# Performance work log

Hardware: AMD Instinct MI355X
Metric: run time of the kernel (lower is better)

Reference implementation:

```python
import jax, jax.numpy as jnp
import numpy as np

N, E, B, ROWS, IN, HID, JKO, FEAT, OH, OUT = 200000, 6400000, 64, 128, 128, 6, 4, 2560, 20, 2

def _leaky(x, s):
    return jnp.where(x >= 0, x, s * x)

def _ln(x, g, b, eps=1e-5):
    mu = jnp.mean(x, -1, keepdims=True)
    v = jnp.mean((x - mu) ** 2, -1, keepdims=True)
    return (x - mu) * jax.lax.rsqrt(v + eps) * g + b

def setup_inputs():
    key = jax.random.key(0)
    ks = jax.random.split(key, 32)
    def w(k, shape, fan_in):
        return jax.random.normal(k, shape, jnp.float32) * (1.0 / np.sqrt(fan_in))
    inp = {
        'x': jax.random.normal(ks[0], (N, IN), jnp.float32),
        'edge_index': jax.random.randint(ks[1], (2, E), 0, N, jnp.int32),
        'batch': jnp.sort(jax.random.randint(ks[2], (N,), 0, B, jnp.int32)),
        'features': jax.random.normal(ks[3], (B, ROWS, FEAT), jnp.float32),
        'one_hot': jax.random.uniform(ks[4], (B, OH), jnp.float32),
        # GATv2Conv params (heads=1)
        'W_l': w(ks[5], (IN, HID), IN), 'b_l': jnp.zeros((HID,)),
        'W_r': w(ks[6], (IN, HID), IN), 'b_r': jnp.zeros((HID,)),
        'att': w(ks[7], (HID,), HID), 'conv_b': jnp.zeros((HID,)),
        # BasicGNN final lin after JK (6 -> 4)
        'jk_W': w(ks[8], (HID, JKO), HID), 'jk_b': jnp.zeros((JKO,)),
        # MLP chain on features
        'l1_W': w(ks[9], (FEAT, 256), FEAT), 'l1_b': jnp.zeros((256,)),
        'ln1_g': jnp.ones((256,)), 'ln1_b': jnp.zeros((256,)),
        'l2_W': w(ks[10], (256, 64), 256), 'l2_b': jnp.zeros((64,)),
        'ln2_g': jnp.ones((64,)), 'ln2_b': jnp.zeros((64,)),
        'l3_W': w(ks[11], (64, 8), 64), 'l3_b': jnp.zeros((8,)),
        'ln3_g': jnp.ones((8,)), 'ln3_b': jnp.zeros((8,)),
        # flattening: rows*8 -> 32
        'fl_W': w(ks[12], (ROWS * 8, 32), ROWS * 8), 'fl_b': jnp.zeros((32,)),
        'ln4_g': jnp.ones((32,)), 'ln4_b': jnp.zeros((32,)),
        # output: 4 + 32 + 20 = 56 -> OUT
        'out_W': w(ks[13], (56, OUT), 56), 'out_b': jnp.zeros((OUT,)),
    }
    return inp

def _forward(x, features, one_hot, W_l, b_l, W_r, b_r, att, conv_b, jk_W, jk_b,
             l1_W, l1_b, ln1_g, ln1_b, l2_W, l2_b, ln2_g, ln2_b, l3_W, l3_b, ln3_g, ln3_b,
             fl_W, fl_b, ln4_g, ln4_b, out_W, out_b, edge_index, batch):
    n = x.shape[0]
    # GATv2Conv, heads=1: separate source/target transforms
    xl = x @ W_l + b_l  # [N,6] source/message features
    xr = x @ W_r + b_r  # [N,6] target features
    loops = jnp.arange(n, dtype=edge_index.dtype)
    src = jnp.concatenate([edge_index[0], loops])  # add self loops
    dst = jnp.concatenate([edge_index[1], loops])
    e = _leaky(xl[src] + xr[dst], 0.2)             # [E+N,6]
    score = e @ att                                 # [E+N]
    m = jax.lax.stop_gradient(jax.ops.segment_max(score, dst, num_segments=n))
    p = jnp.exp(score - m[dst])
    z = jax.ops.segment_sum(p, dst, num_segments=n)
    alpha = p / z[dst]                              # segment softmax over incoming edges
    agg = jax.ops.segment_sum(alpha[:, None] * xl[src], dst, num_segments=n) + conv_b
    x1 = _leaky(agg, 0.01)                          # BasicGNN act ('leakyrelu')
    # JK-LSTM with a single layer collapses to identity (softmax over 1 element)
    h = x1 @ jk_W + jk_b                            # [N,4]
    # global mean pool per graph
    nb = features.shape[0]
    sums = jax.ops.segment_sum(h, batch, num_segments=nb)
    cnt = jax.ops.segment_sum(jnp.ones((n,), h.dtype), batch, num_segments=nb)
    xgcn = sums / jnp.maximum(cnt, 1.0)[:, None]    # [B,4]
    # MLP on features (dropout = identity in eval)
    f = _leaky(_ln(features @ l1_W + l1_b, ln1_g, ln1_b), 0.01)
    f = _leaky(_ln(f @ l2_W + l2_b, ln2_g, ln2_b), 0.01)
    f = _leaky(_ln(f @ l3_W + l3_b, ln3_g, ln3_b), 0.01)  # [B,ROWS,8]
    flat = f.reshape(nb, -1)
    xf = _leaky(_ln(flat @ fl_W + fl_b, ln4_g, ln4_b), 0.01)  # [B,32]
    cat = jnp.concatenate([xgcn, xf, one_hot], axis=1)        # [B,56]
    return cat @ out_W + out_b

def reference(x, features, one_hot, W_l, b_l, W_r, b_r, att, conv_b, jk_W, jk_b,
              l1_W, l1_b, ln1_g, ln1_b, l2_W, l2_b, ln2_g, ln2_b, l3_W, l3_b, ln3_g, ln3_b,
              fl_W, fl_b, ln4_g, ln4_b, out_W, out_b, edge_index, batch):
    return _forward(x, features, one_hot, W_l, b_l, W_r, b_r, att, conv_b, jk_W, jk_b,
                    l1_W, l1_b, ln1_g, ln1_b, l2_W, l2_b, ln2_g, ln2_b, l3_W, l3_b, ln3_g, ln3_b,
                    fl_W, fl_b, ln4_g, ln4_b, out_W, out_b, edge_index, batch)
```

## Files before the change

kernel.cpp:

```cpp
#include <hip/hip_runtime.h>
#include <cstdint>
#include <cstddef>

#define N_NODES 200000
#define N_EDGES 6400000
#define NB      64
#define MROWS   8192
#define FEAT    2560

#define BSZ   256
#define NBK   782
#define EBLK  512
#define ETILE 12500
#define BCAP  8960
#define NXB   768
#define GEMMB 256

typedef __attribute__((ext_vector_type(8))) short bf16x8;
typedef __attribute__((ext_vector_type(4))) float f32x4;

__device__ __forceinline__ unsigned short bf16rne(float f) {
    unsigned u = __builtin_bit_cast(unsigned, f);
    u += 0x7fffu + ((u >> 16) & 1u);
    return (unsigned short)(u >> 16);
}

__device__ __forceinline__ void async_cp16(const void* g, void* l) {
    __builtin_amdgcn_global_load_lds(
        (const __attribute__((address_space(1))) unsigned int*)g,
        (__attribute__((address_space(3))) unsigned int*)l, 16, 0, 0);
}

__device__ __forceinline__ void edge_acc(
    uint4 g, const float* xrd, const float* attv, float& z, float* agg)
{
    float xls[6];
    xls[0] = __builtin_bit_cast(float, g.x << 16);
    xls[1] = __builtin_bit_cast(float, g.x & 0xffff0000u);
    xls[2] = __builtin_bit_cast(float, g.y << 16);
    xls[3] = __builtin_bit_cast(float, g.y & 0xffff0000u);
    xls[4] = __builtin_bit_cast(float, g.z << 16);
    xls[5] = __builtin_bit_cast(float, g.z & 0xffff0000u);
    float sc = 0.f;
#pragma unroll
    for (int j = 0; j < 6; j++) {
        float e = xls[j] + xrd[j];
        e = (e >= 0.f) ? e : 0.2f * e;
        sc += attv[j] * e;
    }
    const float p = __expf(sc);
    z += p;
#pragma unroll
    for (int j = 0; j < 6; j++) agg[j] += p * xls[j];
}


__device__ __forceinline__ void nx_body(
    const int nxi, const int nstride,
    const float* __restrict__ x,
    const float* __restrict__ Wl, const float* __restrict__ bl,
    const float* __restrict__ Wr, const float* __restrict__ br,
    unsigned short* __restrict__ xlb, float* __restrict__ xr)
{
    const int t = threadIdx.x;
    const int l = t & 15;

    float wl[48], wr[48];
#pragma unroll
    for (int q = 0; q < 12; q++) {
        *(float4*)&wl[q * 4] = *(const float4*)(Wl + 48 * l + 4 * q);
        *(float4*)&wr[q * 4] = *(const float4*)(Wr + 48 * l + 4 * q);
    }
    for (int g = nxi; g < N_NODES / 16; g += nstride) {
        const int node = g * 16 + (t >> 4);
        float xv[8];
        *(float4*)&xv[0] = *(const float4*)(x + (size_t)node * 128 + l * 8);
        *(float4*)&xv[4] = *(const float4*)(x + (size_t)node * 128 + l * 8 + 4);

        float al[6] = {}, ar[6] = {};
#pragma unroll
        for (int i = 0; i < 8; i++) {
#pragma unroll
            for (int j = 0; j < 6; j++) {
                al[j] += xv[i] * wl[i * 6 + j];
                ar[j] += xv[i] * wr[i * 6 + j];
            }
        }
#pragma unroll
        for (int off = 8; off >= 1; off >>= 1) {
#pragma unroll
            for (int j = 0; j < 6; j++) {
                al[j] += __shfl_xor(al[j], off);
                ar[j] += __shfl_xor(ar[j], off);
            }
        }
        if (l == 0) {
            union { unsigned short h[8]; uint4 v; } u;
#pragma unroll
            for (int j = 0; j < 6; j++) u.h[j] = bf16rne(al[j] + bl[j]);
            u.h[6] = 0; u.h[7] = 0;
            *(uint4*)(xlb + (size_t)node * 8) = u.v;
            float4 r0; float2 r1;
            r0.x = ar[0] + br[0]; r0.y = ar[1] + br[1];
            r0.z = ar[2] + br[2]; r0.w = ar[3] + br[3];
            r1.x = ar[4] + br[4]; r1.y = ar[5] + br[5];
            *(float4*)(xr + (size_t)node * 8) = r0;
            *(float2*)(xr + (size_t)node * 8 + 4) = r1;
        }
    }
}

__device__ __forceinline__ void eb_body(
    const int bid, char* smem,
    const int* __restrict__ ei, int* __restrict__ cursor, int* __restrict__ pairs)
{
    int* sorted = (int*)smem;
    int* hb     = sorted + ETILE;
    int* cur    = hb + NBK + 1;
    int* gbl    = cur + NBK;
    int* wsum   = gbl + NBK;
    const int t = threadIdx.x;
    const int lane = t & 63, wid = t >> 6;
    const int base = bid * ETILE;

    for (int b = t; b < NBK; b += 256) cur[b] = 0;
    __syncthreads();

    for (int i = t; i < ETILE; i += 256)
        atomicAdd(&cur[ei[N_EDGES + base + i] >> 8], 1);
    __syncthreads();

    int c[4]; int lsum = 0;
#pragma unroll
    for (int q = 0; q < 4; q++) {
        const int b = 4 * t + q;
        c[q] = (b < NBK) ? cur[b] : 0;
        lsum += c[q];
    }
    int v = lsum;
#pragma unroll
    for (int d = 1; d < 64; d <<= 1) {
        const int o = __shfl_up(v, d);
        if (lane >= d) v += o;
    }
    if (lane == 63) wsum[wid] = v;
    __syncthreads();
    int off = 0;
#pragma unroll
    for (int w = 0; w < 3; w++) if (w < wid) off += wsum[w];
    int run = off + v - lsum;

    int mygb[4];
#pragma unroll
    for (int q = 0; q < 4; q++) {
        const int b = 4 * t + q;
        mygb[q] = (b < NBK && c[q] > 0) ? atomicAdd(&cursor[b], c[q]) : 0;
    }

#pragma unroll
    for (int q = 0; q < 4; q++) {
        const int b = 4 * t + q;
        if (b <= NBK) hb[b] = run;
        if (b < NBK) cur[b] = run;
        run += c[q];
    }
    __syncthreads();

    for (int i = t; i < ETILE; i += 256) {
        const int d = ei[N_EDGES + base + i];
        const int s = ei[base + i];
        const int pos = atomicAdd(&cur[d >> 8], 1);
        sorted[pos] = (s << 8) | (d & 255);
    }
#pragma unroll
    for (int q = 0; q < 4; q++) {
        const int b = 4 * t + q;
        if (b < NBK) gbl[b] = mygb[q];
    }
    __syncthreads();

    const int grp = t >> 4, gl = t & 15;
    for (int b = grp; b < NBK; b += 16) {
        const int st = hb[b];
        const int cnt = hb[b + 1] - st;
        int* dst = pairs + b * BCAP + gbl[b];
        for (int i = gl; i < cnt; i += 16)
            dst[i] = sorted[st + i];
    }
}

__device__ __forceinline__ void gemm_l1_body(
    const int bx, const int by, char* smem,
    const float* __restrict__ A, const unsigned short* __restrict__ Bt,
    const float* __restrict__ bias, float* __restrict__ C)
{
    unsigned short (*As)[64 * 64] = (unsigned short(*)[64 * 64])smem;
    unsigned short (*Bs)[128 * 64] =
        (unsigned short(*)[128 * 64])(smem + 2 * 64 * 64 * sizeof(short));
    const int K = FEAT, N = 256;
    const int t = threadIdx.x;
    const int w = t >> 6, l = t & 63;
    const int l15 = l & 15, quad = l >> 4;
    const int wm = (w & 1) * 32, wn = (w >> 1) * 64;
    const int gm0 = bx * 64;
    const int gn0 = by * 128;
    const int r8 = l >> 3;
    const int c8 = (l & 7) ^ r8;
    const int ar = t >> 2;
    const int ac0 = (t & 3) * 2;

    f32x4 acc[2][4];
#pragma unroll
    for (int mt = 0; mt < 2; mt++)
#pragma unroll
        for (int nt = 0; nt < 4; nt++) acc[mt][nt] = (f32x4){0.f, 0.f, 0.f, 0.f};

    const int niter = K / 64;

#pragma unroll
    for (int c = 0; c < 4; c++) {
        const int j = w * 4 + c;
        async_cp16(Bt + (size_t)(gn0 + j * 8 + r8) * K + c8 * 8, &Bs[0][j * 512]);
    }
    {
        const float* src = A + (size_t)(gm0 + ar) * K + ac0 * 8;
        float4 v0 = *(const float4*)src;
        float4 v1 = *(const float4*)(src + 4);
        float4 v2 = *(const float4*)(src + 8);
        float4 v3 = *(const float4*)(src + 12);
        union { unsigned short h[8]; uint4 u; } p0, p1;
        p0.h[0] = bf16rne(v0.x); p0.h[1] = bf16rne(v0.y);
        p0.h[2] = bf16rne(v0.z); p0.h[3] = bf16rne(v0.w);
        p0.h[4] = bf16rne(v1.x); p0.h[5] = bf16rne(v1.y);
        p0.h[6] = bf16rne(v1.z); p0.h[7] = bf16rne(v1.w);
        p1.h[0] = bf16rne(v2.x); p1.h[1] = bf16rne(v2.y);
        p1.h[2] = bf16rne(v2.z); p1.h[3] = bf16rne(v2.w);
        p1.h[4] = bf16rne(v3.x); p1.h[5] = bf16rne(v3.y);
        p1.h[6] = bf16rne(v3.z); p1.h[7] = bf16rne(v3.w);
        *(uint4*)&As[0][ar * 64 + ((ac0 + 0) ^ (ar & 7)) * 8] = p0.u;
        *(uint4*)&As[0][ar * 64 + ((ac0 + 1) ^ (ar & 7)) * 8] = p1.u;
    }

    int p = 0;
    for (int i = 0; i < niter; i++) {
        __syncthreads();
        const bool nxt = (i + 1 < niter);
        float4 v0, v1, v2, v3;
        if (nxt) {
            const int k1 = (i + 1) * 64;
#pragma unroll
            for (int c = 0; c < 4; c++) {
                const int j = w * 4 + c;
                async_cp16(Bt + (size_t)(gn0 + j * 8 + r8) * K + k1 + c8 * 8,
                           &Bs[p ^ 1][j * 512]);
            }
            const float* src = A + (size_t)(gm0 + ar) * K + k1 + ac0 * 8;
            v0 = *(const float4*)src;
            v1 = *(const float4*)(src + 4);
            v2 = *(const float4*)(src + 8);
            v3 = *(const float4*)(src + 12);
        }
#pragma unroll
        for (int kki = 0; kki < 2; kki++) {
            bf16x8 af[2], bfr[4];
#pragma unroll
            for (int mt = 0; mt < 2; mt++) {
                const int m = wm + mt * 16 + l15;
                af[mt] = *(const bf16x8*)&As[p][m * 64 + (((quad + 4 * kki) ^ (m & 7)) * 8)];
            }
#pragma unroll
            for (int nt = 0; nt < 4; nt++) {
                const int n = wn + nt * 16 + l15;
                bfr[nt] = *(const bf16x8*)&Bs[p][n * 64 + (((quad + 4 * kki) ^ (n & 7)) * 8)];
            }
#pragma unroll
            for (int mt = 0; mt < 2; mt++)
#pragma unroll
                for (int nt = 0; nt < 4; nt++)
                    acc[mt][nt] = __builtin_amdgcn_mfma_f32_16x16x32_bf16(
                        af[mt], bfr[nt], acc[mt][nt], 0, 0, 0);
        }
        if (nxt) {
            union { unsigned short h[8]; uint4 u; } p0, p1;
            p0.h[0] = bf16rne(v0.x); p0.h[1] = bf16rne(v0.y);
            p0.h[2] = bf16rne(v0.z); p0.h[3] = bf16rne(v0.w);
            p0.h[4] = bf16rne(v1.x); p0.h[5] = bf16rne(v1.y);
            p0.h[6] = bf16rne(v1.z); p0.h[7] = bf16rne(v1.w);
            p1.h[0] = bf16rne(v2.x); p1.h[1] = bf16rne(v2.y);
            p1.h[2] = bf16rne(v2.z); p1.h[3] = bf16rne(v2.w);
            p1.h[4] = bf16rne(v3.x); p1.h[5] = bf16rne(v3.y);
            p1.h[6] = bf16rne(v3.z); p1.h[7] = bf16rne(v3.w);
            *(uint4*)&As[p ^ 1][ar * 64 + ((ac0 + 0) ^ (ar & 7)) * 8] = p0.u;
            *(uint4*)&As[p ^ 1][ar * 64 + ((ac0 + 1) ^ (ar & 7)) * 8] = p1.u;
        }
        p ^= 1;
    }
#pragma unroll
    for (int nt = 0; nt < 4; nt++) {
        const int col = gn0 + wn + nt * 16 + l15;
        const float bv = bias[col];
#pragma unroll
        for (int mt = 0; mt < 2; mt++)
#pragma unroll
            for (int rr = 0; rr < 4; rr++) {
                const int row = gm0 + wm + mt * 16 + quad * 4 + rr;
                C[(size_t)row * N + col] = acc[mt][nt][rr] + bv;
            }
    }
}


__global__ __launch_bounds__(256) void node_xform(
    const float* __restrict__ x,
    const float* __restrict__ Wl, const float* __restrict__ bl,
    const float* __restrict__ Wr, const float* __restrict__ br,
    unsigned short* __restrict__ xlb, float* __restrict__ xr)
{
    nx_body(blockIdx.x, N_NODES / 16, x, Wl, bl, Wr, br, xlb, xr);
}

__global__ __launch_bounds__(256) void edge_bucket(
    const int* __restrict__ ei, int* __restrict__ cursor, int* __restrict__ pairs)
{
    __shared__ __align__(16) char smem[59408];
    eb_body(blockIdx.x, smem, ei, cursor, pairs);
}

__global__ __launch_bounds__(256) void mfma_gemm_l1(
    const float* __restrict__ A, const unsigned short* __restrict__ Bt,
    const float* __restrict__ bias, float* __restrict__ C)
{
    __shared__ __align__(16) char smem[49152];
    gemm_l1_body(blockIdx.x, blockIdx.y, smem, A, Bt, bias, C);
}

__global__ __launch_bounds__(256) void fused_front(
    const float* __restrict__ x,
    const float* __restrict__ Wl, const float* __restrict__ bl,
    const float* __restrict__ Wr, const float* __restrict__ br,
    unsigned short* __restrict__ xlb, float* __restrict__ xr,
    const int* __restrict__ ei, int* __restrict__ cursor, int* __restrict__ pairs,
    const float* __restrict__ A, const unsigned short* __restrict__ Bt,
    const float* __restrict__ bias, float* __restrict__ C)
{
    __shared__ __align__(16) char smem[59408];
    const int bid = blockIdx.x;
    const int role = bid % 3;
    const int q = bid / 3;
    if (role == 0) {
        eb_body(q, smem, ei, cursor, pairs);
    } else if (role == 1 && q < GEMMB) {
        gemm_l1_body(q & 127, q >> 7, smem, A, Bt, bias, C);
    } else {
        const int nxi = (role == 2) ? q : EBLK + (q - GEMMB);
        nx_body(nxi, NXB, x, Wl, bl, Wr, br, xlb, xr);
    }
}

__global__ __launch_bounds__(256) void bucket_reduce(
    const int* __restrict__ pairs, const int* __restrict__ cursor,
    const unsigned short* __restrict__ xlb, const float* __restrict__ xr,
    const float* __restrict__ att, const float* __restrict__ conv_b,
    const float* __restrict__ jkW, const float* __restrict__ jkb,
    const int* __restrict__ batch,
    float* __restrict__ gsum, float* __restrict__ gcnt)
{
    __shared__ int sorted[BCAP];
    __shared__ int hist[256];
    __shared__ int wtot[4];
    const int t = threadIdx.x;
    const int lane = t & 63, wid = t >> 6;
    const int d0 = blockIdx.x * BSZ + t;

    float xrd[6];
    if (d0 < N_NODES) {
        float4 a = *(const float4*)(xr + (size_t)d0 * 8);
        float2 b = *(const float2*)(xr + (size_t)d0 * 8 + 4);
        xrd[0] = a.x; xrd[1] = a.y; xrd[2] = a.z;
        xrd[3] = a.w; xrd[4] = b.x; xrd[5] = b.y;
    } else {
#pragma unroll
        for (int j = 0; j < 6; j++) xrd[j] = 0.f;
    }
    float attv[6];
#pragma unroll
    for (int j = 0; j < 6; j++) attv[j] = att[j];

    float z = 0.f, agg[6] = {};
    const uint4* xl4 = (const uint4*)xlb;
    const int e0 = blockIdx.x * BCAP;
    const int e1 = e0 + cursor[blockIdx.x];

    for (int c0 = e0; c0 < e1; c0 += BCAP) {
        const int rem = e1 - c0;
        const int cnt_chunk = (rem < BCAP) ? rem : BCAP;
        hist[t] = 0;
        __syncthreads();
        for (int i = t; i < cnt_chunk; i += 256)
            atomicAdd(&hist[pairs[c0 + i] & 255], 1);
        __syncthreads();
        const int h = hist[t];
        int v = h;
#pragma unroll
        for (int d = 1; d < 64; d <<= 1) {
            int o = __shfl_up(v, d);
            if (lane >= d) v += o;
        }
        if (lane == 63) wtot[wid] = v;
        __syncthreads();
        int off = 0;
#pragma unroll
        for (int wv = 0; wv < 3; wv++) if (wv < wid) off += wtot[wv];
        const int my_start = v - h + off;
        const int my_cnt = h;
        __syncthreads();
        hist[t] = my_start;
        __syncthreads();
        for (int i = t; i < cnt_chunk; i += 256) {
            const int pv = pairs[c0 + i];
            const int pos = atomicAdd(&hist[pv & 255], 1);
            sorted[pos] = ((unsigned)pv) >> 8;
        }
        __syncthreads();
        int i = 0;
        for (; i + 4 <= my_cnt; i += 4) {
            const int s0 = sorted[my_start + i];
            const int s1 = sorted[my_start + i + 1];
            const int s2 = sorted[my_start + i + 2];
            const int s3 = sorted[my_start + i + 3];
            const uint4 g0 = xl4[s0], g1 = xl4[s1], g2 = xl4[s2], g3 = xl4[s3];
            edge_acc(g0, xrd, attv, z, agg);
            edge_acc(g1, xrd, attv, z, agg);
            edge_acc(g2, xrd, attv, z, agg);
            edge_acc(g3, xrd, attv, z, agg);
        }
        for (; i < my_cnt; i++) {
            const uint4 g = xl4[sorted[my_start + i]];
            edge_acc(g, xrd, attv, z, agg);
        }
        __syncthreads();
    }

    float hh[4] = {0.f, 0.f, 0.f, 0.f};
    float cw = 0.f;
    int b = 0;
    if (d0 < N_NODES) {
        const uint4 g = xl4[d0];
        float xld[6];
        xld[0] = __builtin_bit_cast(float, g.x << 16);
        xld[1] = __builtin_bit_cast(float, g.x & 0xffff0000u);
        xld[2] = __builtin_bit_cast(float, g.y << 16);
        xld[3] = __builtin_bit_cast(float, g.y & 0xffff0000u);
        xld[4] = __builtin_bit_cast(float, g.z << 16);
        xld[5] = __builtin_bit_cast(float, g.z & 0xffff0000u);
        float sc = 0.f;
#pragma unroll
        for (int j = 0; j < 6; j++) {
            float e = xld[j] + xrd[j];
            e = (e >= 0.f) ? e : 0.2f * e;
            sc += attv[j] * e;
        }
        const float p = __expf(sc);
        const float zz = z + p;
#pragma unroll
        for (int c = 0; c < 4; c++) hh[c] = jkb[c];
#pragma unroll
        for (int j = 0; j < 6; j++) {
            float aj = (agg[j] + p * xld[j]) / zz + conv_b[j];
            aj = (aj >= 0.f) ? aj : 0.01f * aj;
#pragma unroll
            for (int c = 0; c < 4; c++) hh[c] += aj * jkW[j * 4 + c];
        }
        b = batch[d0];
        cw = 1.f;
    }
    const int b0 = __shfl(b, 0);
    if (__all(b == b0)) {
#pragma unroll
        for (int off2 = 32; off2 >= 1; off2 >>= 1) {
#pragma unroll
            for (int c = 0; c < 4; c++) hh[c] += __shfl_xor(hh[c], off2);
            cw += __shfl_xor(cw, off2);
        }
        if (lane == 0 && cw > 0.f) {
#pragma unroll
            for (int c = 0; c < 4; c++) atomicAdd(gsum + b0 * 4 + c, hh[c]);
            atomicAdd(gcnt + b0, cw);
        }
    } else if (cw > 0.f) {
#pragma unroll
        for (int c = 0; c < 4; c++) atomicAdd(gsum + b * 4 + c, hh[c]);
        atomicAdd(gcnt + b, cw);
    }
}

__global__ __launch_bounds__(256) void castT(
    const float* __restrict__ W, unsigned short* __restrict__ Wt, int K, int N)
{
    const int k = blockIdx.x * 256 + threadIdx.x;
    const int n = blockIdx.y;
    if (k < K) Wt[(size_t)n * K + k] = bf16rne(W[(size_t)k * N + n]);
}

__global__ __launch_bounds__(256) void mfma_gemm_l2(
    const unsigned short* __restrict__ Ab, const unsigned short* __restrict__ Bt,
    const float* __restrict__ bias, float* __restrict__ C,
    int M, int N, int K)
{
    __shared__ unsigned short As[32 * 64];
    __shared__ unsigned short Bs[64 * 64];
    const int t = threadIdx.x;
    const int w = t >> 6, l = t & 63;
    const int l15 = l & 15, quad = l >> 4;
    const int gm0 = blockIdx.x * 32;
    const int gn0 = blockIdx.y * 64;
    const int r8 = l >> 3;
    const int c8 = (l & 7) ^ r8;

    f32x4 acc[2];
    acc[0] = (f32x4){0.f, 0.f, 0.f, 0.f};
    acc[1] = (f32x4){0.f, 0.f, 0.f, 0.f};

    for (int k0 = 0; k0 < K; k0 += 64) {
#pragma unroll
        for (int c = 0; c < 2; c++) {
            const int j = w * 2 + c;
            async_cp16(Bt + (size_t)(gn0 + j * 8 + r8) * K + k0 + c8 * 8,
                       &Bs[j * 512]);
        }
        async_cp16(Ab + (size_t)(gm0 + w * 8 + r8) * K + k0 + c8 * 8, &As[w * 512]);
        __syncthreads();
#pragma unroll
        for (int kki = 0; kki < 2; kki++) {
            bf16x8 af[2], bfr;
#pragma unroll
            for (int mt = 0; mt < 2; mt++) {
                const int m = mt * 16 + l15;
                af[mt] = *(const bf16x8*)&As[m * 64 + (((quad + 4 * kki) ^ (m & 7)) * 8)];
            }
            const int n = w * 16 + l15;
            bfr = *(const bf16x8*)&Bs[n * 64 + (((quad + 4 * kki) ^ (n & 7)) * 8)];
#pragma unroll
            for (int mt = 0; mt < 2; mt++)
                acc[mt] = __builtin_amdgcn_mfma_f32_16x16x32_bf16(
                    af[mt], bfr, acc[mt], 0, 0, 0);
        }
        __syncthreads();
    }
    const int col = gn0 + w * 16 + l15;
    const float bv = bias[col];
#pragma unroll
    for (int mt = 0; mt < 2; mt++)
#pragma unroll
        for (int rr = 0; rr < 4; rr++) {
            const int row = gm0 + mt * 16 + quad * 4 + rr;
            C[(size_t)row * N + col] = acc[mt][rr] + bv;
        }
}

__global__ __launch_bounds__(256) void ln_leaky_c256(
    const float* __restrict__ f, unsigned short* __restrict__ out,
    const float* __restrict__ g, const float* __restrict__ b)
{
    const int row = blockIdx.x;
    const int t = threadIdx.x;
    float v = f[(size_t)row * 256 + t];
    float s = v, s2 = v * v;
#pragma unroll
    for (int off = 32; off >= 1; off >>= 1) {
        s += __shfl_xor(s, off);
        s2 += __shfl_xor(s2, off);
    }
    __shared__ float ws[4], ws2[4];
    const int wid = t >> 6, lane = t & 63;
    if (lane == 0) { ws[wid] = s; ws2[wid] = s2; }
    __syncthreads();
    const float S = ws[0] + ws[1] + ws[2] + ws[3];
    const float S2 = ws2[0] + ws2[1] + ws2[2] + ws2[3];
    const float mu = S * (1.0f / 256.0f);
    const float var = S2 * (1.0f / 256.0f) - mu * mu;
    float y = (v - mu) * rsqrtf(var + 1e-5f) * g[t] + b[t];
    y = (y >= 0.f) ? y : 0.01f * y;
    out[(size_t)row * 256 + t] = bf16rne(y);
}

__global__ __launch_bounds__(256) void ln_leaky_c64(
    float* __restrict__ f, const float* __restrict__ g, const float* __restrict__ b)
{
    const int wid = threadIdx.x >> 6, lane = threadIdx.x & 63;
    const int row = blockIdx.x * 4 + wid;
    float v = f[(size_t)row * 64 + lane];
    float s = v, s2 = v * v;
#pragma unroll
    for (int off = 32; off >= 1; off >>= 1) {
        s += __shfl_xor(s, off);
        s2 += __shfl_xor(s2, off);
    }
    const float mu = s * (1.0f / 64.0f);
    const float var = s2 * (1.0f / 64.0f) - mu * mu;
    float y = (v - mu) * rsqrtf(var + 1e-5f) * g[lane] + b[lane];
    f[(size_t)row * 64 + lane] = (y >= 0.f) ? y : 0.01f * y;
}

__global__ __launch_bounds__(256) void l3_ln_leaky(
    const float* __restrict__ f2, const float* __restrict__ W3,
    const float* __restrict__ b3,
    const float* __restrict__ g, const float* __restrict__ b,
    float* __restrict__ f3)
{
    __shared__ float sW[64 * 8];
    const int t = threadIdx.x;
    sW[t] = W3[t]; sW[t + 256] = W3[t + 256];
    __syncthreads();
    const int row = blockIdx.x * 32 + (t >> 3);
    const int c = t & 7;
    float acc = b3[c];
    const float* fr = f2 + (size_t)row * 64;
#pragma unroll 8
    for (int k = 0; k < 64; k++) acc += fr[k] * sW[k * 8 + c];
    float s = acc, s2 = acc * acc;
#pragma unroll
    for (int off = 4; off >= 1; off >>= 1) {
        s += __shfl_xor(s, off);
        s2 += __shfl_xor(s2, off);
    }
    const float mu = s * (1.0f / 8.0f);
    const float var = s2 * (1.0f / 8.0f) - mu * mu;
    float y = (acc - mu) * rsqrtf(var + 1e-5f) * g[c] + b[c];
    f3[(size_t)row * 8 + c] = (y >= 0.f) ? y : 0.01f * y;
}

__global__ __launch_bounds__(256) void flat_ln_leaky(
    const float* __restrict__ f3, const float* __restrict__ W,
    const float* __restrict__ bb,
    const float* __restrict__ g, const float* __restrict__ b,
    float* __restrict__ xf)
{
    __shared__ float sf[1024];
    __shared__ float sp[8][32];
    const int t = threadIdx.x;
    const int gb = blockIdx.x;
    *(float4*)&sf[t * 4] = *(const float4*)(f3 + (size_t)gb * 1024 + t * 4);
    __syncthreads();
    const int c = t & 31, part = t >> 5;
    float acc = 0.f;
    for (int k = part * 128; k < part * 128 + 128; k++) acc += sf[k] * W[k * 32 + c];
    sp[part][c] = acc;
    __syncthreads();
    if (t < 32) {
        float v = bb[t];
#pragma unroll
        for (int p = 0; p < 8; p++) v += sp[p][t];
        float s = v, s2 = v * v;
#pragma unroll
        for (int off = 16; off >= 1; off >>= 1) {
            s += __shfl_xor(s, off);
            s2 += __shfl_xor(s2, off);
        }
        const float mu = s * (1.0f / 32.0f);
        const float var = s2 * (1.0f / 32.0f) - mu * mu;
        float y = (v - mu) * rsqrtf(var + 1e-5f) * g[t] + b[t];
        xf[gb * 32 + t] = (y >= 0.f) ? y : 0.01f * y;
    }
}

__global__ __launch_bounds__(128) void final_out(
    const float* __restrict__ gsum, const float* __restrict__ gcnt,
    const float* __restrict__ xf, const float* __restrict__ onehot,
    const float* __restrict__ Wo, const float* __restrict__ bo,
    float* __restrict__ out)
{
    const int t = threadIdx.x;
    const int gb = t >> 1, o = t & 1;
    float cnt = gcnt[gb];
    cnt = (cnt > 1.f) ? cnt : 1.f;
    float acc = bo[o];
#pragma unroll
    for (int j = 0; j < 4; j++)  acc += (gsum[gb * 4 + j] / cnt) * Wo[j * 2 + o];
#pragma unroll
    for (int j = 0; j < 32; j++) acc += xf[gb * 32 + j] * Wo[(4 + j) * 2 + o];
#pragma unroll
    for (int j = 0; j < 20; j++) acc += onehot[gb * 20 + j] * Wo[(36 + j) * 2 + o];
    out[t] = acc;
}

extern "C" void kernel_launch(void* const* d_in, const int* in_sizes, int n_in,
                              void* d_out, int out_size, void* d_ws, size_t ws_size,
                              hipStream_t stream)
{
    const float* x        = (const float*)d_in[0];
    const int*   ei       = (const int*)d_in[1];
    const int*   batch    = (const int*)d_in[2];
    const float* features = (const float*)d_in[3];
    const float* one_hot  = (const float*)d_in[4];
    const float* W_l   = (const float*)d_in[5];
    const float* b_l   = (const float*)d_in[6];
    const float* W_r   = (const float*)d_in[7];
    const float* b_r   = (const float*)d_in[8];
    const float* att   = (const float*)d_in[9];
    const float* conv_b = (const float*)d_in[10];
    const float* jk_W  = (const float*)d_in[11];
    const float* jk_b  = (const float*)d_in[12];
    const float* l1_W  = (const float*)d_in[13];
    const float* l1_b  = (const float*)d_in[14];
    const float* ln1_g = (const float*)d_in[15];
    const float* ln1_b = (const float*)d_in[16];
    const float* l2_W  = (const float*)d_in[17];
    const float* l2_b  = (const float*)d_in[18];
    const float* ln2_g = (const float*)d_in[19];
    const float* ln2_b = (const float*)d_in[20];
    const float* l3_W  = (const float*)d_in[21];
    const float* l3_b  = (const float*)d_in[22];
    const float* ln3_g = (const float*)d_in[23];
    const float* ln3_b = (const float*)d_in[24];
    const float* fl_W  = (const float*)d_in[25];
    const float* fl_b  = (const float*)d_in[26];
    const float* ln4_g = (const float*)d_in[27];
    const float* ln4_b = (const float*)d_in[28];
    const float* out_W = (const float*)d_in[29];
    const float* out_b = (const float*)d_in[30];
    (void)in_sizes; (void)n_in; (void)out_size;

    float* ws = (float*)d_ws;
    unsigned short* xlb = (unsigned short*)(ws + 0);
    float* xr   = ws + 800000;
    unsigned short* w1t = (unsigned short*)(ws + 2400000);
    unsigned short* w2t = (unsigned short*)(ws + 2727680);
    float* gsum   = ws + 2735872;
    float* gcnt   = ws + 2736128;
    int*   cursor = (int*)(ws + 2736192);
    int* pairs = (int*)(ws + 2737024);

    const bool fuse = ws_size >= (size_t)13481344 * 4;
    float* f1;  unsigned short* f1b;  float* f2;  float* f3;  float* xf;
    if (fuse) {
        f1  = ws + 9743744;
        f1b = (unsigned short*)(ws + 11840896);
        f2  = ws + 12889472;
        f3  = ws + 13413760;
        xf  = ws + 13479296;
    } else {
        f1  = ws + 2737024;
        f1b = (unsigned short*)(ws + 4834176);
        f2  = ws + 5358464;
        f3  = ws + 5882752;
        xf  = ws + 5948288;
    }

    hipMemsetAsync(gsum, 0, 1102 * sizeof(float), stream);

    castT<<<dim3(10, 256), 256, 0, stream>>>(l1_W, w1t, FEAT, 256);
    castT<<<dim3(1, 64), 256, 0, stream>>>(l2_W, w2t, 256, 64);

    if (fuse) {
        fused_front<<<EBLK + GEMMB + NXB, 256, 0, stream>>>(
            x, W_l, b_l, W_r, b_r, xlb, xr,
            ei, cursor, pairs,
            features, w1t, l1_b, f1);
        bucket_reduce<<<NBK, 256, 0, stream>>>(pairs, cursor, xlb, xr, att,
                                               conv_b, jk_W, jk_b, batch,
                                               gsum, gcnt);
    } else {
        node_xform<<<N_NODES / 16, 256, 0, stream>>>(x, W_l, b_l, W_r, b_r,
                                                     xlb, xr);
        edge_bucket<<<EBLK, 256, 0, stream>>>(ei, cursor, pairs);
        bucket_reduce<<<NBK, 256, 0, stream>>>(pairs, cursor, xlb, xr, att,
                                               conv_b, jk_W, jk_b, batch,
                                               gsum, gcnt);
        mfma_gemm_l1<<<dim3(MROWS / 64, 2), 256, 0, stream>>>(
            features, w1t, l1_b, f1);
    }

    ln_leaky_c256<<<MROWS, 256, 0, stream>>>(f1, f1b, ln1_g, ln1_b);
    mfma_gemm_l2<<<dim3(MROWS / 32, 1), 256, 0, stream>>>(
        f1b, w2t, l2_b, f2, MROWS, 64, 256);
    ln_leaky_c64<<<MROWS / 4, 256, 0, stream>>>(f2, ln2_g, ln2_b);
    l3_ln_leaky<<<MROWS / 32, 256, 0, stream>>>(f2, l3_W, l3_b, ln3_g, ln3_b, f3);
    flat_ln_leaky<<<NB, 256, 0, stream>>>(f3, fl_W, fl_b, ln4_g, ln4_b, xf);
    final_out<<<1, 128, 0, stream>>>(gsum, gcnt, xf, one_hot, out_W, out_b, (float*)d_out);
}
```

Baseline: 541.7 us.

## Fuse MLP tail into per-graph blocks co-scheduled with bucket reduce

Replaces the chain of separate LN/GEMM-l2/LN/l3/flatten kernels with one per-graph MLP block that does LN1, the 256x64 layer in fp32 using bf16 weights held in LDS, LN2, l3+LN3 and the flatten layer entirely on-chip. These 64 MLP blocks are interleaved with the bucket_reduce blocks in a single fused_back launch, so the small MLP work overlaps the edge aggregation. This removes several launches and the f1b/f2/f3 round trips through memory. In exchange the l2 GEMM moves from MFMA to scalar shuffle-based FMA, and each MLP block processes 128 rows serially, so a slow MLP block could become the tail of fused_back.

```diff
diff --git a/kernel.cpp b/kernel.cpp
--- a/kernel.cpp
+++ b/kernel.cpp
@@ -15,6 +15,7 @@
 #define BCAP  8960
 #define NXB   768
 #define GEMMB 256
+#define MLPB  64
 
 typedef __attribute__((ext_vector_type(8))) short bf16x8;
 typedef __attribute__((ext_vector_type(4))) float f32x4;
@@ -23,6 +24,10 @@
     unsigned u = __builtin_bit_cast(unsigned, f);
     u += 0x7fffu + ((u >> 16) & 1u);
     return (unsigned short)(u >> 16);
+}
+
+__device__ __forceinline__ float bf16f(unsigned short h) {
+    return __builtin_bit_cast(float, (unsigned)h << 16);
 }
 
 __device__ __forceinline__ void async_cp16(const void* g, void* l) {
@@ -309,55 +314,8 @@
     }
 }
 
-
-__global__ __launch_bounds__(256) void node_xform(
-    const float* __restrict__ x,
-    const float* __restrict__ Wl, const float* __restrict__ bl,
-    const float* __restrict__ Wr, const float* __restrict__ br,
-    unsigned short* __restrict__ xlb, float* __restrict__ xr)
-{
-    nx_body(blockIdx.x, N_NODES / 16, x, Wl, bl, Wr, br, xlb, xr);
-}
-
-__global__ __launch_bounds__(256) void edge_bucket(
-    const int* __restrict__ ei, int* __restrict__ cursor, int* __restrict__ pairs)
-{
-    __shared__ __align__(16) char smem[59408];
-    eb_body(blockIdx.x, smem, ei, cursor, pairs);
-}
-
-__global__ __launch_bounds__(256) void mfma_gemm_l1(
-    const float* __restrict__ A, const unsigned short* __restrict__ Bt,
-    const float* __restrict__ bias, float* __restrict__ C)
-{
-    __shared__ __align__(16) char smem[49152];
-    gemm_l1_body(blockIdx.x, blockIdx.y, smem, A, Bt, bias, C);
-}
-
-__global__ __launch_bounds__(256) void fused_front(
-    const float* __restrict__ x,
-    const float* __restrict__ Wl, const float* __restrict__ bl,
-    const float* __restrict__ Wr, const float* __restrict__ br,
-    unsigned short* __restrict__ xlb, float* __restrict__ xr,
-    const int* __restrict__ ei, int* __restrict__ cursor, int* __restrict__ pairs,
-    const float* __restrict__ A, const unsigned short* __restrict__ Bt,
-    const float* __restrict__ bias, float* __restrict__ C)
-{
-    __shared__ __align__(16) char smem[59408];
-    const int bid = blockIdx.x;
-    const int role = bid % 3;
-    const int q = bid / 3;
-    if (role == 0) {
-        eb_body(q, smem, ei, cursor, pairs);
-    } else if (role == 1 && q < GEMMB) {
-        gemm_l1_body(q & 127, q >> 7, smem, A, Bt, bias, C);
-    } else {
-        const int nxi = (role == 2) ? q : EBLK + (q - GEMMB);
-        nx_body(nxi, NXB, x, Wl, bl, Wr, br, xlb, xr);
-    }
-}
-
-__global__ __launch_bounds__(256) void bucket_reduce(
+__device__ __forceinline__ void br_body(
+    const int bid, char* smem,
     const int* __restrict__ pairs, const int* __restrict__ cursor,
     const unsigned short* __restrict__ xlb, const float* __restrict__ xr,
     const float* __restrict__ att, const float* __restrict__ conv_b,
@@ -365,12 +323,12 @@
     const int* __restrict__ batch,
     float* __restrict__ gsum, float* __restrict__ gcnt)
 {
-    __shared__ int sorted[BCAP];
-    __shared__ int hist[256];
-    __shared__ int wtot[4];
+    int* sorted = (int*)smem;
+    int* hist   = sorted + BCAP;
+    int* wtot   = hist + 256;
     const int t = threadIdx.x;
     const int lane = t & 63, wid = t >> 6;
-    const int d0 = blockIdx.x * BSZ + t;
+    const int d0 = bid * BSZ + t;
 
     float xrd[6];
     if (d0 < N_NODES) {
@@ -388,8 +346,8 @@
 
     float z = 0.f, agg[6] = {};
     const uint4* xl4 = (const uint4*)xlb;
-    const int e0 = blockIdx.x * BCAP;
-    const int e1 = e0 + cursor[blockIdx.x];
+    const int e0 = bid * BCAP;
+    const int e1 = e0 + cursor[bid];
 
     for (int c0 = e0; c0 < e1; c0 += BCAP) {
         const int rem = e1 - c0;
@@ -494,6 +452,229 @@
     }
 }
 
+__device__ __forceinline__ void mlp_body(
+    const int g, char* smem,
+    const float* __restrict__ f1, const unsigned short* __restrict__ w2t,
+    const float* __restrict__ ln1_g, const float* __restrict__ ln1_b,
+    const float* __restrict__ l2_b,
+    const float* __restrict__ ln2_g, const float* __restrict__ ln2_b,
+    const float* __restrict__ l3_W, const float* __restrict__ l3_b,
+    const float* __restrict__ ln3_g, const float* __restrict__ ln3_b,
+    const float* __restrict__ fl_W, const float* __restrict__ fl_b,
+    const float* __restrict__ ln4_g, const float* __restrict__ ln4_b,
+    float* __restrict__ xf)
+{
+    unsigned short* W2 = (unsigned short*)smem;
+    float* f3s = (float*)(smem + 32768);
+    float* sp  = (float*)(smem + 32768 + 4096);
+    const int t = threadIdx.x;
+    const int w = t >> 6, l = t & 63;
+
+    for (int i = t; i < 16384; i += 256) {
+        const int j = i >> 8, k = i & 255;
+        W2[k * 64 + j] = w2t[i];
+    }
+    const float4 g1 = *(const float4*)(ln1_g + 4 * l);
+    const float4 b1 = *(const float4*)(ln1_b + 4 * l);
+    const float bo2 = l2_b[l], g2 = ln2_g[l], b2 = ln2_b[l];
+    float w3r[8];
+    *(float4*)&w3r[0] = *(const float4*)(l3_W + l * 8);
+    *(float4*)&w3r[4] = *(const float4*)(l3_W + l * 8 + 4);
+    float g3[8], b3[8], bo3[8];
+#pragma unroll
+    for (int c = 0; c < 8; c++) {
+        g3[c] = ln3_g[c]; b3[c] = ln3_b[c]; bo3[c] = l3_b[c];
+    }
+    __syncthreads();
+
+    for (int r = w; r < 128; r += 4) {
+        const size_t row = (size_t)g * 128 + r;
+        const float4 v = *(const float4*)(f1 + row * 256 + 4 * l);
+        float s = v.x + v.y + v.z + v.w;
+        float s2 = v.x * v.x + v.y * v.y + v.z * v.z + v.w * v.w;
+#pragma unroll
+        for (int o = 32; o >= 1; o >>= 1) {
+            s += __shfl_xor(s, o);
+            s2 += __shfl_xor(s2, o);
+        }
+        const float mu = s * (1.0f / 256.0f);
+        const float rs = rsqrtf(s2 * (1.0f / 256.0f) - mu * mu + 1e-5f);
+        float y[4];
+        y[0] = (v.x - mu) * rs * g1.x + b1.x;
+        y[1] = (v.y - mu) * rs * g1.y + b1.y;
+        y[2] = (v.z - mu) * rs * g1.z + b1.z;
+        y[3] = (v.w - mu) * rs * g1.w + b1.w;
+#pragma unroll
+        for (int i = 0; i < 4; i++) y[i] = (y[i] >= 0.f) ? y[i] : 0.01f * y[i];
+
+        float acc = bo2;
+#pragma unroll 4
+        for (int k0 = 0; k0 < 64; k0++) {
+            const float yv0 = __shfl(y[0], k0);
+            const float yv1 = __shfl(y[1], k0);
+            const float yv2 = __shfl(y[2], k0);
+            const float yv3 = __shfl(y[3], k0);
+            const int kb = k0 * 256 + l;
+            acc += yv0 * bf16f(W2[kb]);
+            acc += yv1 * bf16f(W2[kb + 64]);
+            acc += yv2 * bf16f(W2[kb + 128]);
+            acc += yv3 * bf16f(W2[kb + 192]);
+        }
+        float s1 = acc, q1 = acc * acc;
+#pragma unroll
+        for (int o = 32; o >= 1; o >>= 1) {
+            s1 += __shfl_xor(s1, o);
+            q1 += __shfl_xor(q1, o);
+        }
+        const float mu2 = s1 * (1.0f / 64.0f);
+        const float rs2 = rsqrtf(q1 * (1.0f / 64.0f) - mu2 * mu2 + 1e-5f);
+        float y2 = (acc - mu2) * rs2 * g2 + b2;
+        y2 = (y2 >= 0.f) ? y2 : 0.01f * y2;
+
+        float p8[8];
+#pragma unroll
+        for (int c = 0; c < 8; c++) p8[c] = y2 * w3r[c];
+#pragma unroll
+        for (int o = 32; o >= 1; o >>= 1)
+#pragma unroll
+            for (int c = 0; c < 8; c++) p8[c] += __shfl_xor(p8[c], o);
+#pragma unroll
+        for (int c = 0; c < 8; c++) p8[c] += bo3[c];
+        float s3 = 0.f;
+#pragma unroll
+        for (int c = 0; c < 8; c++) s3 += p8[c];
+        const float mu3 = s3 * 0.125f;
+        float q3 = 0.f;
+#pragma unroll
+        for (int c = 0; c < 8; c++) { const float d = p8[c] - mu3; q3 += d * d; }
+        const float rs3 = rsqrtf(q3 * 0.125f + 1e-5f);
+        if (l == 0) {
+            float o8[8];
+#pragma unroll
+            for (int c = 0; c < 8; c++) {
+                float yy = (p8[c] - mu3) * rs3 * g3[c] + b3[c];
+                o8[c] = (yy >= 0.f) ? yy : 0.01f * yy;
+            }
+            *(float4*)&f3s[r * 8] = *(float4*)&o8[0];
+            *(float4*)&f3s[r * 8 + 4] = *(float4*)&o8[4];
+        }
+    }
+    __syncthreads();
+
+    const int c = t & 31, part = t >> 5;
+    float facc = 0.f;
+    for (int k = part * 128; k < part * 128 + 128; k++)
+        facc += f3s[k] * fl_W[k * 32 + c];
+    sp[part * 32 + c] = facc;
+    __syncthreads();
+    if (t < 32) {
+        float vv = fl_b[t];
+#pragma unroll
+        for (int p = 0; p < 8; p++) vv += sp[p * 32 + t];
+        float ss = vv, ss2 = vv * vv;
+#pragma unroll
+        for (int o = 16; o >= 1; o >>= 1) {
+            ss += __shfl_xor(ss, o);
+            ss2 += __shfl_xor(ss2, o);
+        }
+        const float mu4 = ss * (1.0f / 32.0f);
+        const float var4 = ss2 * (1.0f / 32.0f) - mu4 * mu4;
+        float yy = (vv - mu4) * rsqrtf(var4 + 1e-5f) * ln4_g[t] + ln4_b[t];
+        xf[g * 32 + t] = (yy >= 0.f) ? yy : 0.01f * yy;
+    }
+}
+
+
+__global__ __launch_bounds__(256) void node_xform(
+    const float* __restrict__ x,
+    const float* __restrict__ Wl, const float* __restrict__ bl,
+    const float* __restrict__ Wr, const float* __restrict__ br,
+    unsigned short* __restrict__ xlb, float* __restrict__ xr)
+{
+    nx_body(blockIdx.x, N_NODES / 16, x, Wl, bl, Wr, br, xlb, xr);
+}
+
+__global__ __launch_bounds__(256) void edge_bucket(
+    const int* __restrict__ ei, int* __restrict__ cursor, int* __restrict__ pairs)
+{
+    __shared__ __align__(16) char smem[59408];
+    eb_body(blockIdx.x, smem, ei, cursor, pairs);
+}
+
+__global__ __launch_bounds__(256) void mfma_gemm_l1(
+    const float* __restrict__ A, const unsigned short* __restrict__ Bt,
+    const float* __restrict__ bias, float* __restrict__ C)
+{
+    __shared__ __align__(16) char smem[49152];
+    gemm_l1_body(blockIdx.x, blockIdx.y, smem, A, Bt, bias, C);
+}
+
+__global__ __launch_bounds__(256) void bucket_reduce(
+    const int* __restrict__ pairs, const int* __restrict__ cursor,
+    const unsigned short* __restrict__ xlb, const float* __restrict__ xr,
+    const float* __restrict__ att, const float* __restrict__ conv_b,
+    const float* __restrict__ jkW, const float* __restrict__ jkb,
+    const int* __restrict__ batch,
+    float* __restrict__ gsum, float* __restrict__ gcnt)
+{
+    __shared__ __align__(16) char smem[36880];
+    br_body(blockIdx.x, smem, pairs, cursor, xlb, xr, att, conv_b, jkW, jkb,
+            batch, gsum, gcnt);
+}
+
+__global__ __launch_bounds__(256) void fused_front(
+    const float* __restrict__ x,
+    const float* __restrict__ Wl, const float* __restrict__ bl,
+    const float* __restrict__ Wr, const float* __restrict__ br,
+    unsigned short* __restrict__ xlb, float* __restrict__ xr,
+    const int* __restrict__ ei, int* __restrict__ cursor, int* __restrict__ pairs,
+    const float* __restrict__ A, const unsigned short* __restrict__ Bt,
+    const float* __restrict__ bias, float* __restrict__ C)
+{
+    __shared__ __align__(16) char smem[59408];
+    const int bid = blockIdx.x;
+    const int role = bid % 3;
+    const int q = bid / 3;
+    if (role == 0) {
+        eb_body(q, smem, ei, cursor, pairs);
+    } else if (role == 1 && q < GEMMB) {
+        gemm_l1_body(q & 127, q >> 7, smem, A, Bt, bias, C);
+    } else {
+        const int nxi = (role == 2) ? q : EBLK + (q - GEMMB);
+        nx_body(nxi, NXB, x, Wl, bl, Wr, br, xlb, xr);
+    }
+}
+
+__global__ __launch_bounds__(256, 4) void fused_back(
+    const int* __restrict__ pairs, const int* __restrict__ cursor,
+    const unsigned short* __restrict__ xlb, const float* __restrict__ xr,
+    const float* __restrict__ att, const float* __restrict__ conv_b,
+    const float* __restrict__ jkW, const float* __restrict__ jkb,
+    const int* __restrict__ batch,
+    float* __restrict__ gsum, float* __restrict__ gcnt,
+    const float* __restrict__ f1, const unsigned short* __restrict__ w2t,
+    const float* __restrict__ ln1_g, const float* __restrict__ ln1_b,
+    const float* __restrict__ l2_b,
+    const float* __restrict__ ln2_g, const float* __restrict__ ln2_b,
+    const float* __restrict__ l3_W, const float* __restrict__ l3_b,
+    const float* __restrict__ ln3_g, const float* __restrict__ ln3_b,
+    const float* __restrict__ fl_W, const float* __restrict__ fl_b,
+    const float* __restrict__ ln4_g, const float* __restrict__ ln4_b,
+    float* __restrict__ xf)
+{
+    __shared__ __align__(16) char smem[37888];
+    const int bid = blockIdx.x;
+    const int q = bid / 13, r = bid % 13;
+    if (r == 0 && q < MLPB) {
+        mlp_body(q, smem, f1, w2t, ln1_g, ln1_b, l2_b, ln2_g, ln2_b,
+                 l3_W, l3_b, ln3_g, ln3_b, fl_W, fl_b, ln4_g, ln4_b, xf);
+    } else {
+        const int brid = bid - ((q < MLPB) ? (q + (r > 0 ? 1 : 0)) : MLPB);
+        br_body(brid, smem, pairs, cursor, xlb, xr, att, conv_b, jkW, jkb,
+                batch, gsum, gcnt);
+    }
+}
+
 __global__ __launch_bounds__(256) void castT(
     const float* __restrict__ W, unsigned short* __restrict__ Wt, int K, int N)
 {
@@ -501,6 +682,7 @@
     const int n = blockIdx.y;
     if (k < K) Wt[(size_t)n * K + k] = bf16rne(W[(size_t)k * N + n]);
 }
+
 
 __global__ __launch_bounds__(256) void mfma_gemm_l2(
     const unsigned short* __restrict__ Ab, const unsigned short* __restrict__ Bt,
@@ -732,20 +914,6 @@
     int* pairs = (int*)(ws + 2737024);
 
     const bool fuse = ws_size >= (size_t)13481344 * 4;
-    float* f1;  unsigned short* f1b;  float* f2;  float* f3;  float* xf;
-    if (fuse) {
-        f1  = ws + 9743744;
-        f1b = (unsigned short*)(ws + 11840896);
-        f2  = ws + 12889472;
-        f3  = ws + 13413760;
-        xf  = ws + 13479296;
-    } else {
-        f1  = ws + 2737024;
-        f1b = (unsigned short*)(ws + 4834176);
-        f2  = ws + 5358464;
-        f3  = ws + 5882752;
-        xf  = ws + 5948288;
-    }
 
     hipMemsetAsync(gsum, 0, 1102 * sizeof(float), stream);
 
@@ -753,14 +921,25 @@
     castT<<<dim3(1, 64), 256, 0, stream>>>(l2_W, w2t, 256, 64);
 
     if (fuse) {
+        float* f1 = ws + 9743744;
+        float* xf = ws + 13479296;
         fused_front<<<EBLK + GEMMB + NXB, 256, 0, stream>>>(
             x, W_l, b_l, W_r, b_r, xlb, xr,
             ei, cursor, pairs,
             features, w1t, l1_b, f1);
-        bucket_reduce<<<NBK, 256, 0, stream>>>(pairs, cursor, xlb, xr, att,
-                                               conv_b, jk_W, jk_b, batch,
-                                               gsum, gcnt);
+        fused_back<<<NBK + MLPB, 256, 0, stream>>>(
+            pairs, cursor, xlb, xr, att, conv_b, jk_W, jk_b, batch,
+            gsum, gcnt,
+            f1, w2t, ln1_g, ln1_b, l2_b, ln2_g, ln2_b,
+            l3_W, l3_b, ln3_g, ln3_b, fl_W, fl_b, ln4_g, ln4_b, xf);
+        final_out<<<1, 128, 0, stream>>>(gsum, gcnt, xf, one_hot, out_W, out_b,
+                                         (float*)d_out);
     } else {
+        float* f1           = ws + 2737024;
+        unsigned short* f1b = (unsigned short*)(ws + 4834176);
+        float* f2           = ws + 5358464;
+        float* f3           = ws + 5882752;
+        float* xf           = ws + 5948288;
         node_xform<<<N_NODES / 16, 256, 0, stream>>>(x, W_l, b_l, W_r, b_r,
                                                      xlb, xr);
         edge_bucket<<<EBLK, 256, 0, stream>>>(ei, cursor, pairs);
@@ -769,13 +948,14 @@
                                                gsum, gcnt);
         mfma_gemm_l1<<<dim3(MROWS / 64, 2), 256, 0, stream>>>(
             features, w1t, l1_b, f1);
-    }
-
-    ln_leaky_c256<<<MROWS, 256, 0, stream>>>(f1, f1b, ln1_g, ln1_b);
-    mfma_gemm_l2<<<dim3(MROWS / 32, 1), 256, 0, stream>>>(
-        f1b, w2t, l2_b, f2, MROWS, 64, 256);
-    ln_leaky_c64<<<MROWS / 4, 256, 0, stream>>>(f2, ln2_g, ln2_b);
-    l3_ln_leaky<<<MROWS / 32, 256, 0, stream>>>(f2, l3_W, l3_b, ln3_g, ln3_b, f3);
-    flat_ln_leaky<<<NB, 256, 0, stream>>>(f3, fl_W, fl_b, ln4_g, ln4_b, xf);
-    final_out<<<1, 128, 0, stream>>>(gsum, gcnt, xf, one_hot, out_W, out_b, (float*)d_out);
-}
+        ln_leaky_c256<<<MROWS, 256, 0, stream>>>(f1, f1b, ln1_g, ln1_b);
+        mfma_gemm_l2<<<dim3(MROWS / 32, 1), 256, 0, stream>>>(
+            f1b, w2t, l2_b, f2, MROWS, 64, 256);
+        ln_leaky_c64<<<MROWS / 4, 256, 0, stream>>>(f2, ln2_g, ln2_b);
+        l3_ln_leaky<<<MROWS / 32, 256, 0, stream>>>(f2, l3_W, l3_b,
+                                                    ln3_g, ln3_b, f3);
+        flat_ln_leaky<<<NB, 256, 0, stream>>>(f3, fl_W, fl_b, ln4_g, ln4_b, xf);
+        final_out<<<1, 128, 0, stream>>>(gsum, gcnt, xf, one_hot, out_W, out_b,
+                                         (float*)d_out);
+    }
+}
```

Result: slower. 651.7 us (+20.3%).
